# Kernel optimization log

Hardware: AMD Instinct MI355X
Metric: run time of the kernel (lower is better)

Reference implementation:

```python
import jax, jax.numpy as jnp
from jax import lax
import numpy as np

B, T, C_IN, H, W = 2, 4, 128, 64, 64
D_MODEL, N_Q, N_POINTS, PATCH, N_LAYERS = 256, 300, 8, 3, 6


def _sine_pos(Hh, Ww, d, temperature=10000.0):
    # mask is all-False, so cumsum of ones -> arange(1..H)/H * 2pi
    two_pi = 2.0 * np.pi
    yn = (jnp.arange(1, Hh + 1, dtype=jnp.float32) / (Hh + 1e-6)) * two_pi
    xn = (jnp.arange(1, Ww + 1, dtype=jnp.float32) / (Ww + 1e-6)) * two_pi
    q = d // 4
    i = jnp.arange(q, dtype=jnp.float32)
    dim_t = temperature ** (2.0 * jnp.floor(i / 2.0) / q)
    py = yn[:, None] / dim_t
    px = xn[:, None] / dim_t
    py = jnp.stack([jnp.sin(py), jnp.cos(py)], axis=-1).reshape(Hh, 2 * q)
    px = jnp.stack([jnp.sin(px), jnp.cos(px)], axis=-1).reshape(Ww, 2 * q)
    pos = jnp.concatenate([
        jnp.broadcast_to(py[:, None, :], (Hh, Ww, 2 * q)),
        jnp.broadcast_to(px[None, :, :], (Hh, Ww, 2 * q)),
    ], axis=-1)
    return jnp.transpose(pos, (2, 0, 1))  # [d,H,W]


def _sample_scale(fmap, ref, ps):
    # fmap [B,C,h,w]; ref [B,nQ,nP,2] in [0,1]. Bilinear grid_sample,
    # padding_mode='border', align_corners=True -> direct gather (no replication).
    Bc, C, h, w = fmap.shape
    half = (ps - 1) / 2.0
    off = jnp.linspace(-half, half, ps, dtype=jnp.float32)
    oy, ox = jnp.meshgrid(off, off, indexing='ij')  # [ps,ps]
    gx = ref[..., 0, None, None] * 2.0 - 1.0 + ox * (2.0 / w)  # [B,nQ,nP,ps,ps]
    gy = ref[..., 1, None, None] * 2.0 - 1.0 + oy * (2.0 / h)
    x = jnp.clip((gx + 1.0) * 0.5 * (w - 1), 0.0, w - 1.0)
    y = jnp.clip((gy + 1.0) * 0.5 * (h - 1), 0.0, h - 1.0)
    x0 = jnp.floor(x); y0 = jnp.floor(y)
    wx = x - x0; wy = y - y0
    x0i = x0.astype(jnp.int32); y0i = y0.astype(jnp.int32)
    x1i = jnp.minimum(x0i + 1, w - 1); y1i = jnp.minimum(y0i + 1, h - 1)

    def per_b(fb, y0b, x0b, y1b, x1b, wxb, wyb):
        v00 = fb[:, y0b, x0b]  # [C,nQ,nP,ps,ps]
        v01 = fb[:, y0b, x1b]
        v10 = fb[:, y1b, x0b]
        v11 = fb[:, y1b, x1b]
        return (v00 * (1 - wxb) * (1 - wyb) + v01 * wxb * (1 - wyb)
                + v10 * (1 - wxb) * wyb + v11 * wxb * wyb)

    out = jax.vmap(per_b)(fmap, y0i, x0i, y1i, x1i, wx, wy)  # [B,C,nQ,nP,ps,ps]
    return jnp.transpose(out, (0, 2, 3, 4, 5, 1))  # [B,nQ,nP,ps,ps,C]


def reference(feat, pred_boxes_init, w_tf, b_tf, w_in, b_in, w_lat, b_lat, w_sm, b_sm,
              q_embed, q_pos, Wq, bq, Wo, bo, Wp1, bp1, Wp2, bp2,
              w_r1, b_r1, w_r2, b_r2, w_b1, b_b1, w_b2, b_b2, w_cls, b_cls):
    Bb, Tt, Cin, Hh, Ww = feat.shape
    d = w_in.shape[0]
    nP = w_r2.shape[0] // 2
    ps = int(round((Wp1.shape[-1] // d) ** 0.5))
    # temporal fuse: Conv3d kernel (3,1,1), padding (1,0,0)
    x = lax.conv_general_dilated(jnp.transpose(feat, (0, 2, 1, 3, 4)), w_tf,
                                 (1, 1, 1), [(1, 1), (0, 0), (0, 0)],
                                 dimension_numbers=('NCDHW', 'OIDHW', 'NCDHW'))
    x = x + b_tf[None, :, None, None, None]
    x = x.mean(axis=2)  # [B,Cin,H,W]
    x = jnp.einsum('bchw,dc->bdhw', x, w_in) + b_in[None, :, None, None]
    x = x + _sine_pos(Hh, Ww, d)[None]
    # FPN over scales {1,2,4}: avg_pool -> 1x1 lateral -> 3x3 smooth
    feats = []
    for i, s in enumerate((1, 2, 4)):
        xi = x if s == 1 else x.reshape(Bb, d, Hh // s, s, Ww // s, s).mean(axis=(3, 5))
        xi = jnp.einsum('bchw,oc->bohw', xi, w_lat[i]) + b_lat[i][None, :, None, None]
        xi = lax.conv_general_dilated(xi, w_sm[i], (1, 1), [(1, 1), (1, 1)],
                                      dimension_numbers=('NCHW', 'OIHW', 'NCHW'))
        xi = xi + b_sm[i][None, :, None, None]
        feats.append(xi)
    nQ = q_embed.shape[0]
    queries = jnp.broadcast_to((q_embed + q_pos)[None], (Bb, nQ, d))
    boxes = pred_boxes_init
    inv_sqrt_d = 1.0 / float(np.sqrt(d))
    for l in range(Wq.shape[0]):
        h1 = jax.nn.relu(jnp.einsum('bqd,od->bqo', queries, w_r1) + b_r1)
        ro = jnp.tanh(jnp.einsum('bqd,od->bqo', h1, w_r2) + b_r2)
        ro = ro.reshape(Bb, nQ, nP, 2) * 0.5
        ref = jnp.clip(boxes[:, :, None, :2] + ro, 0.0, 1.0)
        sampled = jnp.concatenate([_sample_scale(f, ref, ps) for f in feats], axis=2)
        sampled = sampled[:, :, :nP]  # truncate multi-scale concat back to nP
        flat = sampled.reshape(Bb, nQ, nP, ps * ps * d)
        pv = jax.nn.relu(jnp.einsum('bqpi,oi->bqpo', flat, Wp1[l]) + bp1[l])
        pv = jnp.einsum('bqpd,od->bqpo', pv, Wp2[l]) + bp2[l]
        kv = pv.mean(axis=2)  # [B,nP_q,d] -> [B,nQ,d]
        q = jnp.einsum('bqd,od->bqo', queries, Wq[l]) + bq[l]
        attn = jax.nn.softmax(jnp.einsum('bqd,bkd->bqk', q, kv) * inv_sqrt_d, axis=-1)
        out = jnp.einsum('bqk,bkd->bqd', attn, kv)
        queries = queries + (jnp.einsum('bqd,od->bqo', out, Wo[l]) + bo[l])
        hb = jax.nn.relu(jnp.einsum('bqd,od->bqo', queries, w_b1) + b_b1)
        delta = jax.nn.sigmoid(jnp.einsum('bqd,od->bqo', hb, w_b2) + b_b2)
        boxes = jnp.clip(boxes + 0.1 * jnp.tanh(delta - 0.5), 0.0, 1.0)
    logits = (jnp.einsum('bqd,od->bqo', queries, w_cls) + b_cls)[..., 0]
    return logits, boxes


def setup_inputs() -> dict:
    key = jax.random.key(0)
    keys = iter(jax.random.split(key, 48))

    def nrm(shape, s=0.02):
        return jax.random.normal(next(keys), shape, dtype=jnp.float32) * s

    inp = {
        'feat': jax.random.normal(next(keys), (B, T, C_IN, H, W), dtype=jnp.float32),
        'pred_boxes_init': jax.random.uniform(next(keys), (B, N_Q, 4), dtype=jnp.float32),
        'w_tf': nrm((C_IN, C_IN, 3, 1, 1)), 'b_tf': jnp.zeros((C_IN,), jnp.float32),
        'w_in': nrm((D_MODEL, C_IN)), 'b_in': jnp.zeros((D_MODEL,), jnp.float32),
        'w_lat': nrm((3, D_MODEL, D_MODEL)), 'b_lat': jnp.zeros((3, D_MODEL), jnp.float32),
        'w_sm': nrm((3, D_MODEL, D_MODEL, 3, 3)), 'b_sm': jnp.zeros((3, D_MODEL), jnp.float32),
        'q_embed': nrm((N_Q, D_MODEL), 1.0), 'q_pos': nrm((N_Q, D_MODEL), 1.0),
        'Wq': nrm((N_LAYERS, D_MODEL, D_MODEL)), 'bq': jnp.zeros((N_LAYERS, D_MODEL), jnp.float32),
        'Wo': nrm((N_LAYERS, D_MODEL, D_MODEL)), 'bo': jnp.zeros((N_LAYERS, D_MODEL), jnp.float32),
        'Wp1': nrm((N_LAYERS, D_MODEL, PATCH * PATCH * D_MODEL)), 'bp1': jnp.zeros((N_LAYERS, D_MODEL), jnp.float32),
        'Wp2': nrm((N_LAYERS, D_MODEL, D_MODEL)), 'bp2': jnp.zeros((N_LAYERS, D_MODEL), jnp.float32),
        'w_r1': nrm((D_MODEL, D_MODEL)), 'b_r1': jnp.zeros((D_MODEL,), jnp.float32),
        'w_r2': nrm((2 * N_POINTS, D_MODEL)), 'b_r2': jnp.zeros((2 * N_POINTS,), jnp.float32),
        'w_b1': nrm((D_MODEL, D_MODEL)), 'b_b1': jnp.zeros((D_MODEL,), jnp.float32),
        'w_b2': nrm((4, D_MODEL)), 'b_b2': jnp.zeros((4,), jnp.float32),
        'w_cls': nrm((1, D_MODEL)), 'b_cls': jnp.zeros((1,), jnp.float32),
    }
    return inp
```

## Files before the change

### kernel.cpp

```cpp
#include <hip/hip_runtime.h>
#include <hip/hip_bf16.h>
#include <math.h>

#define BB 2
#define TT 4
#define CIN 128
#define DM 256
#define NQ 300
#define NP 8
#define PS 3
#define NL 6
#define HW 4096
#define KP 2304

typedef __attribute__((ext_vector_type(8))) short short8;
typedef __attribute__((ext_vector_type(4))) short short4_t;
typedef __attribute__((ext_vector_type(4))) float f32x4;
typedef unsigned short ushort_t;

static __device__ __forceinline__ ushort_t f2bf(float f) {
  __hip_bfloat16 h = __float2bfloat16(f);
  return *reinterpret_cast<ushort_t*>(&h);
}
static __device__ __forceinline__ float bf2f(ushort_t u) {
  return __uint_as_float(((unsigned)u) << 16);
}

__global__ void k_prep(const float* __restrict__ w_in, const float* __restrict__ w_lat,
                       const float* __restrict__ w_b1,
                       const float* __restrict__ w_r1, const float* __restrict__ Wp1,
                       ushort_t* __restrict__ win_bf, ushort_t* __restrict__ wlat_bf,
                       ushort_t* __restrict__ wb1_bf,
                       ushort_t* __restrict__ wr1_bf, ushort_t* __restrict__ wp1_bf,
                       const float* __restrict__ w_tf, ushort_t* __restrict__ tct,
                       const float* __restrict__ w_sm, ushort_t* __restrict__ wsm_bf,
                       const float* __restrict__ Wp2, const float* __restrict__ Wo,
                       const float* __restrict__ bq, const float* __restrict__ bp2,
                       const float* __restrict__ bo,
                       float* __restrict__ bqt, float* __restrict__ bfuse,
                       uint4* __restrict__ x2p_zero,
                       const float* __restrict__ b_tf, const float* __restrict__ b_in,
                       float* __restrict__ bias_comb,
                       const float* __restrict__ qe, const float* __restrict__ qp,
                       const float* __restrict__ pb, float* __restrict__ queries,
                       ushort_t* __restrict__ qbf, float* __restrict__ boxes,
                       const float* __restrict__ feat, ushort_t* __restrict__ featT) {
  __shared__ float ldsF[64][65];
  float* bt = &ldsF[0][0];
  int b = blockIdx.x, t = threadIdx.x;
  if (b < 3680) {
    int i = b * 256 + t;
    const float* s; ushort_t* d; int base;
    if (i < 8192)         { s = w_in;  d = win_bf;  base = 0; }
    else if (i < 24576)   { s = w_lat; d = wlat_bf; base = 8192; }
    else if (i < 40960)   { s = w_b1;  d = wb1_bf;  base = 24576; }
    else if (i < 57344)   { s = w_r1;  d = wr1_bf;  base = 40960; }
    else                  { s = Wp1;   d = wp1_bf;  base = 57344; }
    int j = i - base;
    float4 v = ((const float4*)s)[j];
    d[j * 4 + 0] = f2bf(v.x);
    d[j * 4 + 1] = f2bf(v.y);
    d[j * 4 + 2] = f2bf(v.z);
    d[j * 4 + 3] = f2bf(v.w);
  } else if (b < 3936) {
    int i = (b - 3680) * 256 + t;
    int k = i >> 7, c = i & 127;
    int u = k >> 7, ci = k & 127;
    const float* wp = w_tf + ((size_t)(c * 128 + ci)) * 3;
    float w0 = wp[0], w1 = wp[1], w2 = wp[2];
    float coef = (u == 0) ? (w0 + w1) : (u == 3) ? (w1 + w2) : (w0 + w1 + w2);
    tct[(size_t)k * 128 + c] = f2bf(0.25f * coef);
  } else if (b < 6240) {
    int i = (b - 3936) * 256 + t;
    int n = i / KP;
    int r = i - n * KP;
    int tp = r >> 8, c = r & 255;
    wsm_bf[i] = f2bf(w_sm[((size_t)(n * 256 + c)) * 9 + tp]);
  } else if (b < 6252) {
    int i = (b - 6240) * 256 + t;
    if (i < 1536) {
      int l = i >> 8, d = i & 255;
      float a = 0.f;
      for (int o = 0; o < 256; ++o)
        a += bq[l * 256 + o] * Wp2[((size_t)(l * 256 + o)) * 256 + d];
      bqt[i] = a;
    } else {
      int j = i - 1536;
      int l = j >> 8, o2 = j & 255;
      float a = bo[l * 256 + o2];
      for (int o = 0; o < 256; ++o)
        a += bp2[l * 256 + o] * Wo[((size_t)(l * 256 + o2)) * 256 + o];
      bfuse[j] = a;
    }
  } else if (b < 7341) {
    int j = (b - 6252) * 256 + t;
    if (j < 278784) x2p_zero[j] = make_uint4(0u, 0u, 0u, 0u);
  } else if (b < 7342) {
    int d = t;
    if (d < 128) bt[d] = b_tf[d];
    __syncthreads();
    float a = b_in[d];
    for (int c = 0; c < 128; ++c) a += w_in[d * 128 + c] * bt[c];
    bias_comb[d] = a;
  } else if (b < 7942) {
    int i = (b - 7342) * 256 + t;
    if (i < BB * NQ * DM) {
      int rd = i % (NQ * DM);
      float v = qe[rd] + qp[rd];
      queries[i] = v;
      qbf[i] = f2bf(v);
    }
    if (i < BB * NQ * 4) boxes[i] = pb[i];
  } else {
    int idx = b - 7942;
    int gs = idx & 127;
    int k0 = (idx >> 7) * 64;
    int bb = gs >> 6;
    int s0 = (gs & 63) * 64;
    int kk = t >> 2, sc0 = (t & 3) * 16;
    {
      int k = k0 + kk;
      int u = k >> 7, ci = k & 127;
      const float* src = feat + (((size_t)(bb * 4 + u) * 128 + ci) << 12) + s0 + sc0;
#pragma unroll
      for (int j = 0; j < 4; ++j) {
        float4 v = *(const float4*)(src + j * 4);
        ldsF[kk][sc0 + j * 4 + 0] = v.x;
        ldsF[kk][sc0 + j * 4 + 1] = v.y;
        ldsF[kk][sc0 + j * 4 + 2] = v.z;
        ldsF[kk][sc0 + j * 4 + 3] = v.w;
      }
    }
    __syncthreads();
#pragma unroll
    for (int p = 0; p < 2; ++p) {
      int idx2 = p * 256 + t;
      int s_l = idx2 >> 3, kc = (idx2 & 7) * 8;
      short8 v;
#pragma unroll
      for (int j = 0; j < 8; ++j) v[j] = (short)f2bf(ldsF[kc + j][s_l]);
      *(short8*)(featT + (size_t)(bb * 4096 + s0 + s_l) * 512 + k0 + kc) = v;
    }
  }
}

__global__ __launch_bounds__(256) void k_wcompose(const float* __restrict__ Wp2,
                                                  const float* __restrict__ Wq,
                                                  const float* __restrict__ Wo,
                                                  ushort_t* __restrict__ wqt,
                                                  ushort_t* __restrict__ wfuseT) {
  __shared__ ushort_t As[64 * 36];
  __shared__ ushort_t Bs[64 * 36];
  int z = blockIdx.z, l = z % 6;
  const float* Asrc = Wp2 + (size_t)l * 65536;
  const float* Bsrc = ((z < 6) ? Wq : Wo) + (size_t)l * 65536;
  ushort_t* C = ((z < 6) ? wqt : wfuseT) + (size_t)l * 65536;
  bool btr = (z < 6);
  int tid = threadIdx.x;
  int bm = blockIdx.x * 64, bn = blockIdx.y * 64;
  int w = tid >> 6, lane = tid & 63;
  int wm = (w & 1) * 32, wn = (w >> 1) * 32;
  int q = lane >> 4, ml = lane & 15;
  f32x4 acc[2][2] = {};
  int oo = tid >> 3, mg = (tid & 7) * 8;
  int nr = tid >> 2, kg = (tid & 3) * 8;
  for (int k0 = 0; k0 < 256; k0 += 32) {
    {
      const float* sp = Asrc + (size_t)(k0 + oo) * 256 + bm + mg;
      float4 f0 = *(const float4*)sp;
      float4 f1 = *(const float4*)(sp + 4);
      ushort_t* dst = As + oo;
      dst[(mg + 0) * 36] = f2bf(f0.x); dst[(mg + 1) * 36] = f2bf(f0.y);
      dst[(mg + 2) * 36] = f2bf(f0.z); dst[(mg + 3) * 36] = f2bf(f0.w);
      dst[(mg + 4) * 36] = f2bf(f1.x); dst[(mg + 5) * 36] = f2bf(f1.y);
      dst[(mg + 6) * 36] = f2bf(f1.z); dst[(mg + 7) * 36] = f2bf(f1.w);
    }
    if (btr) {
      const float* sp = Bsrc + (size_t)(k0 + oo) * 256 + bn + mg;
      float4 f0 = *(const float4*)sp;
      float4 f1 = *(const float4*)(sp + 4);
      ushort_t* dst = Bs + oo;
      dst[(mg + 0) * 36] = f2bf(f0.x); dst[(mg + 1) * 36] = f2bf(f0.y);
      dst[(mg + 2) * 36] = f2bf(f0.z); dst[(mg + 3) * 36] = f2bf(f0.w);
      dst[(mg + 4) * 36] = f2bf(f1.x); dst[(mg + 5) * 36] = f2bf(f1.y);
      dst[(mg + 6) * 36] = f2bf(f1.z); dst[(mg + 7) * 36] = f2bf(f1.w);
    } else {
      const float* sp = Bsrc + (size_t)(bn + nr) * 256 + k0 + kg;
      float4 f0 = *(const float4*)sp;
      float4 f1 = *(const float4*)(sp + 4);
      short8 v;
      v[0] = (short)f2bf(f0.x); v[1] = (short)f2bf(f0.y);
      v[2] = (short)f2bf(f0.z); v[3] = (short)f2bf(f0.w);
      v[4] = (short)f2bf(f1.x); v[5] = (short)f2bf(f1.y);
      v[6] = (short)f2bf(f1.z); v[7] = (short)f2bf(f1.w);
      *(short8*)(Bs + nr * 36 + kg) = v;
    }
    __syncthreads();
    short8 a0 = *(const short8*)(As + (wm + ml) * 36 + q * 8);
    short8 a1 = *(const short8*)(As + (wm + 16 + ml) * 36 + q * 8);
    short8 b0 = *(const short8*)(Bs + (wn + ml) * 36 + q * 8);
    short8 b1 = *(const short8*)(Bs + (wn + 16 + ml) * 36 + q * 8);
    acc[0][0] = __builtin_amdgcn_mfma_f32_16x16x32_bf16(a0, b0, acc[0][0], 0, 0, 0);
    acc[0][1] = __builtin_amdgcn_mfma_f32_16x16x32_bf16(a0, b1, acc[0][1], 0, 0, 0);
    acc[1][0] = __builtin_amdgcn_mfma_f32_16x16x32_bf16(a1, b0, acc[1][0], 0, 0, 0);
    acc[1][1] = __builtin_amdgcn_mfma_f32_16x16x32_bf16(a1, b1, acc[1][1], 0, 0, 0);
    __syncthreads();
  }
#pragma unroll
  for (int i = 0; i < 2; ++i)
#pragma unroll
    for (int j = 0; j < 2; ++j) {
      int cn = bn + wn + j * 16 + ml;
#pragma unroll
      for (int r = 0; r < 4; ++r) {
        int rm = bm + wm + i * 16 + q * 4 + r;
        C[(size_t)rm * 256 + cn] = f2bf(acc[i][j][r]);
      }
    }
}

__global__ __launch_bounds__(256) void k_feat2(const ushort_t* __restrict__ featT,
                                               const ushort_t* __restrict__ wcomb,
                                               const float* __restrict__ biasc,
                                               ushort_t* __restrict__ xcl) {
  __shared__ ushort_t As[32 * 72];
  __shared__ ushort_t Bs[64 * 72];
  __shared__ float dimt_s[256];
  int tid = threadIdx.x;
  {
    int dd = tid & 127;
    int ii = dd >> 1;
    dimt_s[tid] = powf(10000.0f, (2.0f * (float)(ii >> 1)) / 64.0f);
  }
  int bm = blockIdx.x * 32, bn = blockIdx.y * 64;
  int w = tid >> 6, lane = tid & 63;
  int wm = (w & 1) * 16, wn = (w >> 1) * 32;
  int q = lane >> 4, ml = lane & 15;
  int sra = tid >> 3, sca = (tid & 7) * 8;
  int srb = tid >> 2, scb = (tid & 3) * 16;
  const ushort_t* Ag = featT + (size_t)(bm + sra) * 512 + sca;
  const ushort_t* Wg = wcomb + (size_t)(bn + srb) * 512 + scb;
  f32x4 acc[2] = {};
  short8 av = *(const short8*)Ag;
  short8 wv0 = *(const short8*)Wg;
  short8 wv1 = *(const short8*)(Wg + 8);
  for (int k0 = 0; k0 < 512; k0 += 64) {
    *(short8*)(As + sra * 72 + sca) = av;
    *(short8*)(Bs + srb * 72 + scb) = wv0;
    *(short8*)(Bs + srb * 72 + scb + 8) = wv1;
    __syncthreads();
    if (k0 + 64 < 512) {
      av = *(const short8*)(Ag + k0 + 64);
      wv0 = *(const short8*)(Wg + k0 + 64);
      wv1 = *(const short8*)(Wg + k0 + 72);
    }
#pragma unroll
    for (int h = 0; h < 2; ++h) {
      int kc = h * 32 + q * 8;
      short8 a = *(const short8*)(As + (wm + ml) * 72 + kc);
      short8 b0 = *(const short8*)(Bs + (wn + ml) * 72 + kc);
      short8 b1 = *(const short8*)(Bs + (wn + 16 + ml) * 72 + kc);
      acc[0] = __builtin_amdgcn_mfma_f32_16x16x32_bf16(a, b0, acc[0], 0, 0, 0);
      acc[1] = __builtin_amdgcn_mfma_f32_16x16x32_bf16(a, b1, acc[1], 0, 0, 0);
    }
    __syncthreads();
  }
  const float FKT = 6.28318530717958647692f / 64.000001f;
#pragma unroll
  for (int j = 0; j < 2; ++j) {
    int cn = bn + wn + j * 16 + ml;
    float dimt = dimt_s[cn];
    float bC = biasc[cn];
    bool isx = cn >= 128;
    bool isc = cn & 1;
#pragma unroll
    for (int r = 0; r < 4; ++r) {
      int rm = bm + wm + q * 4 + r;
      int s = rm & 4095;
      int y = s >> 6, x = s & 63;
      float ang = (float)((isx ? x : y) + 1) * FKT / dimt;
      float pos = isc ? cosf(ang) : sinf(ang);
      xcl[(size_t)rm * 256 + cn] = f2bf(acc[j][r] + bC + pos);
    }
  }
}

template <int ACT, int OUTMODE, int MG>
__global__ __launch_bounds__(256) void k_gemm_bf16(const ushort_t* __restrict__ A,
                                                   const ushort_t* __restrict__ W,
                                                   const float* __restrict__ bias,
                                                   const float* __restrict__ res,
                                                   float* __restrict__ Cf,
                                                   ushort_t* __restrict__ Cb,
                                                   int M, int N, int K,
                                                   const ushort_t* __restrict__ W2,
                                                   const float* __restrict__ bias2,
                                                   const ushort_t* __restrict__ W3,
                                                   const float* __restrict__ bias3) {
  __shared__ ushort_t As[64 * 72];
  __shared__ ushort_t Bs[64 * 72];
  int tid = threadIdx.x;
  int bm = blockIdx.x * 64, bn = blockIdx.y * 64;
  int w = tid >> 6, lane = tid & 63;
  int wm = (w & 1) * 32, wn = (w >> 1) * 32;
  int q = lane >> 4, ml = lane & 15;
  f32x4 acc[2][2] = {};
  int srow = tid >> 2, scol = (tid & 3) * 16;
  int ga = bm + srow;
  if (MG) ga = min(ga, M - 1);
  const ushort_t* Ag = A + (size_t)ga * K + scol;
  const ushort_t* Wg;
  if (OUTMODE == 7) {
    int seg = bn >> 8;
    const ushort_t* Wb = (seg == 0) ? W : ((seg == 1) ? W2 : W3);
    Wg = Wb + (size_t)((bn & 255) + srow) * K + scol;
  } else if (OUTMODE == 4) {
    const ushort_t* Wb = (bn < 256) ? W : W2;
    Wg = Wb + (size_t)((bn & 255) + srow) * K + scol;
  } else {
    Wg = W + (size_t)(bn + srow) * K + scol;
  }
  short8 av0 = *(const short8*)(Ag);
  short8 av1 = *(const short8*)(Ag + 8);
  short8 wv0 = *(const short8*)(Wg);
  short8 wv1 = *(const short8*)(Wg + 8);
  for (int k0 = 0; k0 < K; k0 += 64) {
    *(short8*)(As + srow * 72 + scol) = av0;
    *(short8*)(As + srow * 72 + scol + 8) = av1;
    *(short8*)(Bs + srow * 72 + scol) = wv0;
    *(short8*)(Bs + srow * 72 + scol + 8) = wv1;
    __syncthreads();
    if (k0 + 64 < K) {
      av0 = *(const short8*)(Ag + k0 + 64);
      av1 = *(const short8*)(Ag + k0 + 72);
      wv0 = *(const short8*)(Wg + k0 + 64);
      wv1 = *(const short8*)(Wg + k0 + 72);
    }
#pragma unroll
    for (int h = 0; h < 2; ++h) {
      int kc = h * 32 + q * 8;
      short8 a0 = *(const short8*)(As + (wm + ml) * 72 + kc);
      short8 a1 = *(const short8*)(As + (wm + 16 + ml) * 72 + kc);
      short8 b0 = *(const short8*)(Bs + (wn + ml) * 72 + kc);
      short8 b1 = *(const short8*)(Bs + (wn + 16 + ml) * 72 + kc);
      acc[0][0] = __builtin_amdgcn_mfma_f32_16x16x32_bf16(a0, b0, acc[0][0], 0, 0, 0);
      acc[0][1] = __builtin_amdgcn_mfma_f32_16x16x32_bf16(a0, b1, acc[0][1], 0, 0, 0);
      acc[1][0] = __builtin_amdgcn_mfma_f32_16x16x32_bf16(a1, b0, acc[1][0], 0, 0, 0);
      acc[1][1] = __builtin_amdgcn_mfma_f32_16x16x32_bf16(a1, b1, acc[1][1], 0, 0, 0);
    }
    __syncthreads();
  }
#pragma unroll
  for (int i = 0; i < 2; ++i) {
#pragma unroll
    for (int j = 0; j < 2; ++j) {
      int cn = bn + wn + j * 16 + ml;
      float bsv;
      if (OUTMODE == 7) {
        int seg = cn >> 8;
        bsv = ((seg == 0) ? bias : ((seg == 1) ? bias2 : bias3))[cn & 255];
      } else if (OUTMODE == 4) {
        bsv = ((cn < 256) ? bias : bias2)[cn & 255];
      } else {
        bsv = bias ? bias[cn] : 0.f;
      }
#pragma unroll
      for (int r = 0; r < 4; ++r) {
        int rm = bm + wm + i * 16 + q * 4 + r;
        if (MG && rm >= M) continue;
        float v = acc[i][j][r] + bsv;
        if (OUTMODE == 0) {
          if (ACT == 1) v = fmaxf(v, 0.f);
          Cf[(size_t)rm * N + cn] = v;
        } else if (OUTMODE == 1) {
          int b = rm >> 12, rem = rm & 4095;
          int y = rem >> 6, xx = rem & 63;
          Cb[(((size_t)(b * 66 + y + 1)) * 66 + xx + 1) * 256 + cn] = f2bf(v);
        } else if (OUTMODE == 4) {
          if (cn < 256) Cf[(size_t)rm * 256 + cn] = fmaxf(v, 0.f);
          else Cb[(size_t)rm * 256 + (cn & 255)] = f2bf(v);
        } else if (OUTMODE == 6) {
          Cb[(size_t)rm * N + cn] = f2bf(v);
        } else if (OUTMODE == 7) {
          if (cn < 256) Cf[(size_t)rm * 256 + cn] = fmaxf(v, 0.f);
          else if (cn < 512) ((float*)Cb)[(size_t)rm * 256 + (cn & 255)] = fmaxf(v, 0.f);
          else ((ushort_t*)res)[(size_t)rm * 256 + (cn & 255)] = f2bf(v);
        }
      }
    }
  }
}

__global__ __launch_bounds__(256) void k_wp1_split(const ushort_t* __restrict__ A,
                                                   const ushort_t* __restrict__ W,
                                                   ushort_t* __restrict__ part) {
  __shared__ ushort_t As[64 * 72];
  __shared__ ushort_t Bs[64 * 72];
  int tid = threadIdx.x;
  int bm = blockIdx.x * 64, bn = blockIdx.y * 64;
  int kz = blockIdx.z * 768;
  int w = tid >> 6, lane = tid & 63;
  int wm = (w & 1) * 32, wn = (w >> 1) * 32;
  int q = lane >> 4, ml = lane & 15;
  int srow = tid >> 2, scol = (tid & 3) * 16;
  const ushort_t* Ag = A + (size_t)(bm + srow) * KP + kz + scol;
  const ushort_t* Wg = W + (size_t)(bn + srow) * KP + kz + scol;
  f32x4 acc[2][2] = {};
  short8 av0 = *(const short8*)(Ag);
  short8 av1 = *(const short8*)(Ag + 8);
  short8 wv0 = *(const short8*)(Wg);
  short8 wv1 = *(const short8*)(Wg + 8);
  for (int k0 = 0; k0 < 768; k0 += 64) {
    *(short8*)(As + srow * 72 + scol) = av0;
    *(short8*)(As + srow * 72 + scol + 8) = av1;
    *(short8*)(Bs + srow * 72 + scol) = wv0;
    *(short8*)(Bs + srow * 72 + scol + 8) = wv1;
    __syncthreads();
    if (k0 + 64 < 768) {
      av0 = *(const short8*)(Ag + k0 + 64);
      av1 = *(const short8*)(Ag + k0 + 72);
      wv0 = *(const short8*)(Wg + k0 + 64);
      wv1 = *(const short8*)(Wg + k0 + 72);
    }
#pragma unroll
    for (int h = 0; h < 2; ++h) {
      int kc = h * 32 + q * 8;
      short8 a0 = *(const short8*)(As + (wm + ml) * 72 + kc);
      short8 a1 = *(const short8*)(As + (wm + 16 + ml) * 72 + kc);
      short8 b0 = *(const short8*)(Bs + (wn + ml) * 72 + kc);
      short8 b1 = *(const short8*)(Bs + (wn + 16 + ml) * 72 + kc);
      acc[0][0] = __builtin_amdgcn_mfma_f32_16x16x32_bf16(a0, b0, acc[0][0], 0, 0, 0);
      acc[0][1] = __builtin_amdgcn_mfma_f32_16x16x32_bf16(a0, b1, acc[0][1], 0, 0, 0);
      acc[1][0] = __builtin_amdgcn_mfma_f32_16x16x32_bf16(a1, b0, acc[1][0], 0, 0, 0);
      acc[1][1] = __builtin_amdgcn_mfma_f32_16x16x32_bf16(a1, b1, acc[1][1], 0, 0, 0);
    }
    __syncthreads();
  }
  ushort_t* pz = part + (size_t)blockIdx.z * 4800 * 256;
#pragma unroll
  for (int i = 0; i < 2; ++i)
#pragma unroll
    for (int j = 0; j < 2; ++j) {
      int cn = bn + wn + j * 16 + ml;
#pragma unroll
      for (int r = 0; r < 4; ++r) {
        int rm = bm + wm + i * 16 + q * 4 + r;
        pz[(size_t)rm * 256 + cn] = f2bf(acc[i][j][r]);
      }
    }
}

__global__ __launch_bounds__(256) void k_wp1_reduce(const ushort_t* __restrict__ part,
                                                    const float* __restrict__ bias,
                                                    ushort_t* __restrict__ pvm) {
  int row = blockIdx.x;
  int d = threadIdx.x;
  float b = bias[d];
  float s = 0.f;
#pragma unroll
  for (int p = 0; p < 8; ++p) {
    size_t idx = (size_t)(row * 8 + p) * 256 + d;
    float v = bf2f(part[idx]) + bf2f(part[idx + (size_t)4800 * 256]) +
              bf2f(part[idx + (size_t)2 * 4800 * 256]) + b;
    s += fmaxf(v, 0.f);
  }
  pvm[(size_t)row * 256 + d] = f2bf(s * 0.125f);
}

__global__ __launch_bounds__(256) void k_conv3(const ushort_t* __restrict__ x2p,
                                               const ushort_t* __restrict__ wsm,
                                               const float* __restrict__ bsm,
                                               ushort_t* __restrict__ fcl) {
  __shared__ ushort_t As[32 * 72];
  __shared__ ushort_t Bs[64 * 72];
  int tid = threadIdx.x;
  int bm = blockIdx.x * 32, bn = blockIdx.y * 64;
  int w = tid >> 6, lane = tid & 63;
  int wm = (w & 1) * 16, wn = (w >> 1) * 32;
  int q = lane >> 4, ml = lane & 15;
  int sra = tid >> 3, sca = (tid & 7) * 8;
  int srb = tid >> 2, scb = (tid & 3) * 16;
  int sA = bm + sra;
  int b = sA >> 12, rem = sA & 4095;
  size_t pbase = ((size_t)(b * 66 + (rem >> 6)) * 66 + (rem & 63)) * 256;
  const ushort_t* Wg = wsm + (size_t)(bn + srb) * KP + scb;
  auto loadA = [&](int k0) {
    int ka = k0 + sca;
    int t9 = ka >> 8;
    int ky = t9 / 3, kx = t9 - ky * 3;
    return *(const short8*)(x2p + pbase + (size_t)(ky * 66 + kx) * 256 + (ka & 255));
  };
  f32x4 acc[2] = {};
  short8 av = loadA(0);
  short8 wv0 = *(const short8*)(Wg);
  short8 wv1 = *(const short8*)(Wg + 8);
  for (int k0 = 0; k0 < KP; k0 += 64) {
    *(short8*)(As + sra * 72 + sca) = av;
    *(short8*)(Bs + srb * 72 + scb) = wv0;
    *(short8*)(Bs + srb * 72 + scb + 8) = wv1;
    __syncthreads();
    if (k0 + 64 < KP) {
      av = loadA(k0 + 64);
      wv0 = *(const short8*)(Wg + k0 + 64);
      wv1 = *(const short8*)(Wg + k0 + 72);
    }
#pragma unroll
    for (int h = 0; h < 2; ++h) {
      int kc = h * 32 + q * 8;
      short8 a = *(const short8*)(As + (wm + ml) * 72 + kc);
      short8 b0 = *(const short8*)(Bs + (wn + ml) * 72 + kc);
      short8 b1 = *(const short8*)(Bs + (wn + 16 + ml) * 72 + kc);
      acc[0] = __builtin_amdgcn_mfma_f32_16x16x32_bf16(a, b0, acc[0], 0, 0, 0);
      acc[1] = __builtin_amdgcn_mfma_f32_16x16x32_bf16(a, b1, acc[1], 0, 0, 0);
    }
    __syncthreads();
  }
#pragma unroll
  for (int j = 0; j < 2; ++j) {
    int cn = bn + wn + j * 16 + ml;
    float bsv = bsm[cn];
#pragma unroll
    for (int r = 0; r < 4; ++r) {
      int rm = bm + wm + q * 4 + r;
      fcl[(size_t)rm * 256 + cn] = f2bf(acc[j][r] + bsv);
    }
  }
}

__global__ __launch_bounds__(256) void k_sample(const ushort_t* __restrict__ fcl,
                                                const float* __restrict__ h1,
                                                const float* __restrict__ w_r2,
                                                const float* __restrict__ b_r2,
                                                const float* __restrict__ boxesIn,
                                                float* __restrict__ boxesOut,
                                                const float* __restrict__ hb,
                                                const float* __restrict__ w_b2,
                                                const float* __restrict__ b_b2,
                                                ushort_t* __restrict__ flat) {
  __shared__ float pr[8];
  __shared__ float bc2[2];
  __shared__ float nb2[2];
  int blk = blockIdx.x;
  int row = blk >> 3, p = blk & 7;
  int b = row / NQ;
  int tid = threadIdx.x;
  int w = tid >> 6, lane = tid & 63;
  if (hb) {
    float4 hv = *(const float4*)(hb + (size_t)row * 256 + lane * 4);
    float4 wv = *(const float4*)(w_b2 + (size_t)w * 256 + lane * 4);
    float aa = hv.x * wv.x + hv.y * wv.y + hv.z * wv.z + hv.w * wv.w;
#pragma unroll
    for (int s = 32; s > 0; s >>= 1) aa += __shfl_down(aa, s, 64);
    if (lane == 0) {
      aa += b_b2[w];
      float delta = 1.0f / (1.0f + expf(-aa));
      float v = boxesIn[row * 4 + w] + 0.1f * tanhf(delta - 0.5f);
      v = fminf(fmaxf(v, 0.f), 1.f);
      if (w < 2) nb2[w] = v;
      if (p == 0) boxesOut[row * 4 + w] = v;
    }
  } else if (tid < 2) {
    nb2[tid] = boxesIn[row * 4 + tid];
  }
  float h = h1[(size_t)row * 256 + tid];
  float px = h * w_r2[(size_t)(2 * p) * 256 + tid];
  float py = h * w_r2[(size_t)(2 * p + 1) * 256 + tid];
#pragma unroll
  for (int s = 32; s > 0; s >>= 1) {
    px += __shfl_down(px, s, 64);
    py += __shfl_down(py, s, 64);
  }
  if (lane == 0) { pr[w * 2] = px; pr[w * 2 + 1] = py; }
  __syncthreads();
  if (tid == 0) {
    float sx = pr[0] + pr[2] + pr[4] + pr[6] + b_r2[2 * p];
    float sy = pr[1] + pr[3] + pr[5] + pr[7] + b_r2[2 * p + 1];
    float rx = nb2[0] + 0.5f * tanhf(sx);
    float ry = nb2[1] + 0.5f * tanhf(sy);
    bc2[0] = fminf(fmaxf(rx, 0.f), 1.f);
    bc2[1] = fminf(fmaxf(ry, 0.f), 1.f);
  }
  __syncthreads();
  float rx = bc2[0], ry = bc2[1];
  int c = tid;
  const ushort_t* fb = fcl + (size_t)b * HW * DM;
  ushort_t* op = flat + (size_t)blk * KP;
#pragma unroll
  for (int jy = 0; jy < 3; ++jy) {
    float yy = (ry + (float)(jy - 1) * (1.0f / 64.0f)) * 63.0f;
    yy = fminf(fmaxf(yy, 0.f), 63.0f);
    float y0f = floorf(yy);
    float wy = yy - y0f;
    int y0 = (int)y0f;
    int y1 = min(y0 + 1, 63);
#pragma unroll
    for (int jx = 0; jx < 3; ++jx) {
      float xx = (rx + (float)(jx - 1) * (1.0f / 64.0f)) * 63.0f;
      xx = fminf(fmaxf(xx, 0.f), 63.0f);
      float x0f = floorf(xx);
      float wx = xx - x0f;
      int x0 = (int)x0f;
      int x1 = min(x0 + 1, 63);
      float v00 = bf2f(fb[(y0 * 64 + x0) * DM + c]);
      float v01 = bf2f(fb[(y0 * 64 + x1) * DM + c]);
      float v10 = bf2f(fb[(y1 * 64 + x0) * DM + c]);
      float v11 = bf2f(fb[(y1 * 64 + x1) * DM + c]);
      float v = v00 * (1.f - wx) * (1.f - wy) + v01 * wx * (1.f - wy) +
                v10 * (1.f - wx) * wy + v11 * wx * wy;
      op[(jy * 3 + jx) * DM + c] = f2bf(v);
    }
  }
}

__global__ __launch_bounds__(256) void k_attn(const ushort_t* __restrict__ qt,
                                              const ushort_t* __restrict__ pvm,
                                              const ushort_t* __restrict__ wfT,
                                              const float* __restrict__ bfuse_l,
                                              float* __restrict__ queries,
                                              ushort_t* __restrict__ qbf) {
  __shared__ float qs[256];
  __shared__ float sc[512];
  __shared__ float red[256];
  __shared__ float pr4[1024];
  int row = blockIdx.x;
  int b = row / NQ;
  int tid = threadIdx.x;
  qs[tid] = bf2f(qt[(size_t)row * DM + tid]);
  __syncthreads();
  const ushort_t* kvB = pvm + (size_t)b * NQ * DM;
#pragma unroll
  for (int s2 = 0; s2 < 2; ++s2) {
    int k = tid + s2 * 256;
    float v = -1e30f;
    if (k < NQ) {
      const ushort_t* kp = kvB + (size_t)k * DM;
      float a = 0.f;
#pragma unroll
      for (int d = 0; d < 256; d += 8) {
        short8 k8 = *(const short8*)(kp + d);
        const float* qd = qs + d;
        a += bf2f((ushort_t)k8[0]) * qd[0];
        a += bf2f((ushort_t)k8[1]) * qd[1];
        a += bf2f((ushort_t)k8[2]) * qd[2];
        a += bf2f((ushort_t)k8[3]) * qd[3];
        a += bf2f((ushort_t)k8[4]) * qd[4];
        a += bf2f((ushort_t)k8[5]) * qd[5];
        a += bf2f((ushort_t)k8[6]) * qd[6];
        a += bf2f((ushort_t)k8[7]) * qd[7];
      }
      v = a * (1.0f / 16.0f);
    }
    sc[k] = v;
  }
  __syncthreads();
  red[tid] = fmaxf(sc[tid], sc[tid + 256]);
  __syncthreads();
  for (int st = 128; st > 0; st >>= 1) {
    if (tid < st) red[tid] = fmaxf(red[tid], red[tid + st]);
    __syncthreads();
  }
  float mx = red[0];
  __syncthreads();
  float e0 = (tid < NQ) ? expf(sc[tid] - mx) : 0.f;
  float e1 = (tid + 256 < NQ) ? expf(sc[tid + 256] - mx) : 0.f;
  sc[tid] = e0;
  sc[tid + 256] = e1;
  red[tid] = e0 + e1;
  __syncthreads();
  for (int st = 128; st > 0; st >>= 1) {
    if (tid < st) red[tid] += red[tid + st];
    __syncthreads();
  }
  float inv = 1.0f / red[0];
  __syncthreads();
  float acc = 0.f;
#pragma unroll 4
  for (int k = 0; k < NQ; ++k)
    acc += sc[k] * bf2f(kvB[(size_t)k * DM + tid]);
  qs[tid] = acc * inv;
  __syncthreads();
  int oq = (tid & 63) * 4, dq = (tid >> 6) * 64;
  float a0 = 0.f, a1 = 0.f, a2 = 0.f, a3 = 0.f;
  const ushort_t* wp = wfT + (size_t)dq * 256 + oq;
#pragma unroll 8
  for (int dd = 0; dd < 64; ++dd) {
    float cc = qs[dq + dd];
    short4_t wv = *(const short4_t*)(wp + (size_t)dd * 256);
    a0 += cc * bf2f((ushort_t)wv[0]);
    a1 += cc * bf2f((ushort_t)wv[1]);
    a2 += cc * bf2f((ushort_t)wv[2]);
    a3 += cc * bf2f((ushort_t)wv[3]);
  }
  float* pb4 = pr4 + (tid >> 6) * 256 + oq;
  pb4[0] = a0; pb4[1] = a1; pb4[2] = a2; pb4[3] = a3;
  __syncthreads();
  float v = pr4[tid] + pr4[256 + tid] + pr4[512 + tid] + pr4[768 + tid] +
            bfuse_l[tid] + queries[(size_t)row * DM + tid];
  queries[(size_t)row * DM + tid] = v;
  qbf[(size_t)row * DM + tid] = f2bf(v);
}

__global__ __launch_bounds__(256) void k_boxf(const float* __restrict__ hb,
                                              const float* __restrict__ w_b2,
                                              const float* __restrict__ b_b2,
                                              float* __restrict__ boxes,
                                              int last,
                                              const float* __restrict__ queries,
                                              const float* __restrict__ w_cls,
                                              const float* __restrict__ b_cls,
                                              float* __restrict__ out) {
  __shared__ float nb[4];
  int row = blockIdx.x;
  int tid = threadIdx.x;
  int j = tid >> 6, lane = tid & 63;
  float4 hv = *(const float4*)(hb + (size_t)row * 256 + lane * 4);
  float4 wv = *(const float4*)(w_b2 + (size_t)j * 256 + lane * 4);
  float aa = hv.x * wv.x + hv.y * wv.y + hv.z * wv.z + hv.w * wv.w;
#pragma unroll
  for (int s = 32; s > 0; s >>= 1) aa += __shfl_down(aa, s, 64);
  if (lane == 0) {
    aa += b_b2[j];
    float delta = 1.0f / (1.0f + expf(-aa));
    float v = boxes[row * 4 + j] + 0.1f * tanhf(delta - 0.5f);
    v = fminf(fmaxf(v, 0.f), 1.f);
    boxes[row * 4 + j] = v;
    nb[j] = v;
  }
  if (last) {
    __syncthreads();
    if (j == 0) {
      float4 qv = *(const float4*)(queries + (size_t)row * 256 + lane * 4);
      float4 cv = *(const float4*)(w_cls + lane * 4);
      float a2 = qv.x * cv.x + qv.y * cv.y + qv.z * cv.z + qv.w * cv.w;
#pragma unroll
      for (int s = 32; s > 0; s >>= 1) a2 += __shfl_down(a2, s, 64);
      if (lane == 0) out[row] = a2 + b_cls[0];
    } else if (j == 1 && lane < 4) {
      out[600 + row * 4 + lane] = nb[lane];
    }
  }
}

extern "C" void kernel_launch(void* const* d_in, const int* in_sizes, int n_in,
                              void* d_out, int out_size, void* d_ws, size_t ws_size,
                              hipStream_t stream) {
  const float* feat   = (const float*)d_in[0];
  const float* pb     = (const float*)d_in[1];
  const float* w_tf   = (const float*)d_in[2];
  const float* b_tf   = (const float*)d_in[3];
  const float* w_in   = (const float*)d_in[4];
  const float* b_in   = (const float*)d_in[5];
  const float* w_lat  = (const float*)d_in[6];
  const float* b_lat  = (const float*)d_in[7];
  const float* w_sm   = (const float*)d_in[8];
  const float* b_sm   = (const float*)d_in[9];
  const float* q_embed= (const float*)d_in[10];
  const float* q_pos  = (const float*)d_in[11];
  const float* Wq     = (const float*)d_in[12];
  const float* bq     = (const float*)d_in[13];
  const float* Wo     = (const float*)d_in[14];
  const float* bo     = (const float*)d_in[15];
  const float* Wp1    = (const float*)d_in[16];
  const float* bp1    = (const float*)d_in[17];
  const float* Wp2    = (const float*)d_in[18];
  const float* bp2    = (const float*)d_in[19];
  const float* w_r1   = (const float*)d_in[20];
  const float* b_r1   = (const float*)d_in[21];
  const float* w_r2   = (const float*)d_in[22];
  const float* b_r2   = (const float*)d_in[23];
  const float* w_b1   = (const float*)d_in[24];
  const float* b_b1   = (const float*)d_in[25];
  const float* w_b2   = (const float*)d_in[26];
  const float* b_b2   = (const float*)d_in[27];
  const float* w_cls  = (const float*)d_in[28];
  const float* b_cls  = (const float*)d_in[29];
  float* out = (float*)d_out;

  float* ws = (float*)d_ws;
  size_t off = 0;
  auto alloc = [&](size_t n) { float* p = ws + off; off += n; return p; };
  ushort_t* flat    = (ushort_t*)alloc(5529600);
  ushort_t* part    = (ushort_t*)alloc(1843200);
  ushort_t* featT   = (ushort_t*)alloc(2097152);
  ushort_t* xcl     = (ushort_t*)alloc(1048576);
  ushort_t* x2p     = (ushort_t*)alloc(1115136);
  ushort_t* fcl     = (ushort_t*)alloc(1048576);
  ushort_t* wcomb   = (ushort_t*)alloc(65536);
  ushort_t* tct     = (ushort_t*)alloc(32768);
  ushort_t* win_bf  = (ushort_t*)alloc(16384);
  float*    biasc   = alloc(256);
  ushort_t* wlat_bf = (ushort_t*)alloc(32768);
  ushort_t* wsm_bf  = (ushort_t*)alloc(294912);
  ushort_t* wp1_bf  = (ushort_t*)alloc(1769472);
  ushort_t* wb1_bf  = (ushort_t*)alloc(32768);
  ushort_t* wr1_bf  = (ushort_t*)alloc(32768);
  ushort_t* wqt_bf  = (ushort_t*)alloc(196608);
  ushort_t* wfuseT  = (ushort_t*)alloc(196608);
  float*    bqt     = alloc(1536);
  float*    bfuse   = alloc(1536);
  float* queries = alloc(153600);
  ushort_t* qbf  = (ushort_t*)alloc(76800);
  float* h1      = alloc(153600);
  ushort_t* qt   = (ushort_t*)alloc(76800);
  float* hb      = alloc(153600);
  ushort_t* pvm  = (ushort_t*)alloc(76800);
  float* boxesA  = alloc(2400);
  float* boxesB  = alloc(2400);
  (void)ws_size; (void)in_sizes; (void)n_in; (void)out_size;

  k_prep<<<8966, 256, 0, stream>>>(w_in, w_lat, w_b1, w_r1, Wp1,
                                   win_bf, wlat_bf, wb1_bf, wr1_bf, wp1_bf,
                                   w_tf, tct, w_sm, wsm_bf,
                                   Wp2, Wo, bq, bp2, bo, bqt, bfuse,
                                   (uint4*)x2p, b_tf, b_in, biasc,
                                   q_embed, q_pos, pb, queries, qbf, boxesA,
                                   feat, featT);
  k_gemm_bf16<0, 6, 0><<<dim3(4, 8), 256, 0, stream>>>(win_bf, tct, nullptr, nullptr,
                                                       nullptr, wcomb, 256, 512, 128,
                                                       nullptr, nullptr, nullptr, nullptr);
  k_wcompose<<<dim3(4, 4, 12), 256, 0, stream>>>(Wp2, Wq, Wo, wqt_bf, wfuseT);

  k_feat2<<<dim3(256, 4), 256, 0, stream>>>(featT, wcomb, biasc, xcl);
  k_gemm_bf16<0, 1, 0><<<dim3(128, 4), 256, 0, stream>>>(xcl, wlat_bf, b_lat, nullptr,
                                                         nullptr, x2p, BB * HW, 256, 256,
                                                         nullptr, nullptr, nullptr, nullptr);
  k_conv3<<<dim3(256, 4), 256, 0, stream>>>(x2p, wsm_bf, b_sm, fcl);

  const int M6 = BB * NQ;
  const int Mp = BB * NQ * NP;
  dim3 g600w((M6 + 63) / 64, 8);
  dim3 g600m((M6 + 63) / 64, 12);
  dim3 gsk(Mp / 64, 4, 3);

  k_gemm_bf16<0, 4, 1><<<g600w, 256, 0, stream>>>(qbf, wr1_bf, b_r1, nullptr, h1,
                                                  qt, M6, 512, 256,
                                                  wqt_bf, bqt, nullptr, nullptr);
  float* bcur = boxesA;
  float* bnext = boxesB;
  for (int l = 0; l < NL; ++l) {
    const float* hbp = (l == 0) ? nullptr : hb;
    k_sample<<<Mp, 256, 0, stream>>>(fcl, h1, w_r2, b_r2, bcur, bnext,
                                     hbp, w_b2, b_b2, flat);
    if (l > 0) { float* tmp = bcur; bcur = bnext; bnext = tmp; }
    k_wp1_split<<<gsk, 256, 0, stream>>>(flat, wp1_bf + (size_t)l * 256 * KP, part);
    k_wp1_reduce<<<600, 256, 0, stream>>>(part, bp1 + (size_t)l * DM, pvm);
    k_attn<<<M6, 256, 0, stream>>>(qt, pvm, wfuseT + (size_t)l * 65536,
                                   bfuse + l * 256, queries, qbf);
    int ln = (l + 1) % NL;
    k_gemm_bf16<0, 7, 1><<<g600m, 256, 0, stream>>>(qbf, wb1_bf, b_b1, (const float*)qt,
                                                    hb, (ushort_t*)h1, M6, 768, 256,
                                                    wr1_bf, b_r1,
                                                    wqt_bf + (size_t)ln * 65536,
                                                    bqt + ln * 256);
  }
  k_boxf<<<M6, 256, 0, stream>>>(hb, w_b2, b_b2, bcur, 1,
                                 queries, w_cls, b_cls, out);
}
```

Baseline: 673.9 us.

## Fold lateral 1x1 conv into 3x3 smoothing weights and vectorize sampling

Composes the lateral 1x1 projection weights into each tap of the 3x3 smoothing conv (new k_convcompose), so the separate lateral GEMM launch and its intermediate buffer go away. The lateral bias is propagated through a per-tap bias table applied with border-aware masking in the conv epilogue, and k_feat2 writes straight into the padded layout. Separately, k_sample now has each thread handle four channels with vector loads and splits the nine patch positions across warps. Composing the weights rounds an extra bf16 product, which may change numerics slightly.

Measured after the change: 694.8 us. 1.03x slower.

```diff
diff --git a/kernel.cpp b/kernel.cpp
--- a/kernel.cpp
+++ b/kernel.cpp
@@ -26,10 +26,10 @@
   return __uint_as_float(((unsigned)u) << 16);
 }
 
-__global__ void k_prep(const float* __restrict__ w_in, const float* __restrict__ w_lat,
+__global__ void k_prep(const float* __restrict__ w_in,
                        const float* __restrict__ w_b1,
                        const float* __restrict__ w_r1, const float* __restrict__ Wp1,
-                       ushort_t* __restrict__ win_bf, ushort_t* __restrict__ wlat_bf,
+                       ushort_t* __restrict__ win_bf,
                        ushort_t* __restrict__ wb1_bf,
                        ushort_t* __restrict__ wr1_bf, ushort_t* __restrict__ wp1_bf,
                        const float* __restrict__ w_tf, ushort_t* __restrict__ tct,
@@ -38,7 +38,8 @@
                        const float* __restrict__ bq, const float* __restrict__ bp2,
                        const float* __restrict__ bo,
                        float* __restrict__ bqt, float* __restrict__ bfuse,
-                       uint4* __restrict__ x2p_zero,
+                       const float* __restrict__ b_lat, float* __restrict__ T9,
+                       uint4* __restrict__ xclp_zero,
                        const float* __restrict__ b_tf, const float* __restrict__ b_in,
                        float* __restrict__ bias_comb,
                        const float* __restrict__ qe, const float* __restrict__ qp,
@@ -48,62 +49,68 @@
   __shared__ float ldsF[64][65];
   float* bt = &ldsF[0][0];
   int b = blockIdx.x, t = threadIdx.x;
-  if (b < 3680) {
+  if (b < 3616) {
     int i = b * 256 + t;
     const float* s; ushort_t* d; int base;
     if (i < 8192)         { s = w_in;  d = win_bf;  base = 0; }
-    else if (i < 24576)   { s = w_lat; d = wlat_bf; base = 8192; }
-    else if (i < 40960)   { s = w_b1;  d = wb1_bf;  base = 24576; }
-    else if (i < 57344)   { s = w_r1;  d = wr1_bf;  base = 40960; }
-    else                  { s = Wp1;   d = wp1_bf;  base = 57344; }
+    else if (i < 24576)   { s = w_b1;  d = wb1_bf;  base = 8192; }
+    else if (i < 40960)   { s = w_r1;  d = wr1_bf;  base = 24576; }
+    else                  { s = Wp1;   d = wp1_bf;  base = 40960; }
     int j = i - base;
     float4 v = ((const float4*)s)[j];
     d[j * 4 + 0] = f2bf(v.x);
     d[j * 4 + 1] = f2bf(v.y);
     d[j * 4 + 2] = f2bf(v.z);
     d[j * 4 + 3] = f2bf(v.w);
-  } else if (b < 3936) {
-    int i = (b - 3680) * 256 + t;
+  } else if (b < 3872) {
+    int i = (b - 3616) * 256 + t;
     int k = i >> 7, c = i & 127;
     int u = k >> 7, ci = k & 127;
     const float* wp = w_tf + ((size_t)(c * 128 + ci)) * 3;
     float w0 = wp[0], w1 = wp[1], w2 = wp[2];
     float coef = (u == 0) ? (w0 + w1) : (u == 3) ? (w1 + w2) : (w0 + w1 + w2);
     tct[(size_t)k * 128 + c] = f2bf(0.25f * coef);
-  } else if (b < 6240) {
-    int i = (b - 3936) * 256 + t;
+  } else if (b < 6176) {
+    int i = (b - 3872) * 256 + t;
     int n = i / KP;
     int r = i - n * KP;
     int tp = r >> 8, c = r & 255;
     wsm_bf[i] = f2bf(w_sm[((size_t)(n * 256 + c)) * 9 + tp]);
-  } else if (b < 6252) {
-    int i = (b - 6240) * 256 + t;
+  } else if (b < 6197) {
+    int i = (b - 6176) * 256 + t;
     if (i < 1536) {
       int l = i >> 8, d = i & 255;
       float a = 0.f;
       for (int o = 0; o < 256; ++o)
         a += bq[l * 256 + o] * Wp2[((size_t)(l * 256 + o)) * 256 + d];
       bqt[i] = a;
-    } else {
+    } else if (i < 3072) {
       int j = i - 1536;
       int l = j >> 8, o2 = j & 255;
       float a = bo[l * 256 + o2];
       for (int o = 0; o < 256; ++o)
         a += bp2[l * 256 + o] * Wo[((size_t)(l * 256 + o2)) * 256 + o];
       bfuse[j] = a;
-    }
-  } else if (b < 7341) {
-    int j = (b - 6252) * 256 + t;
-    if (j < 278784) x2p_zero[j] = make_uint4(0u, 0u, 0u, 0u);
-  } else if (b < 7342) {
+    } else {
+      int j = i - 3072;
+      int tap = j >> 8, n = j & 255;
+      float a = 0.f;
+      for (int c = 0; c < 256; ++c)
+        a += w_sm[((size_t)(n * 256 + c)) * 9 + tap] * b_lat[c];
+      T9[j] = a;
+    }
+  } else if (b < 7286) {
+    int j = (b - 6197) * 256 + t;
+    if (j < 278784) xclp_zero[j] = make_uint4(0u, 0u, 0u, 0u);
+  } else if (b < 7287) {
     int d = t;
     if (d < 128) bt[d] = b_tf[d];
     __syncthreads();
     float a = b_in[d];
     for (int c = 0; c < 128; ++c) a += w_in[d * 128 + c] * bt[c];
     bias_comb[d] = a;
-  } else if (b < 7942) {
-    int i = (b - 7342) * 256 + t;
+  } else if (b < 7887) {
+    int i = (b - 7287) * 256 + t;
     if (i < BB * NQ * DM) {
       int rd = i % (NQ * DM);
       float v = qe[rd] + qp[rd];
@@ -112,7 +119,7 @@
     }
     if (i < BB * NQ * 4) boxes[i] = pb[i];
   } else {
-    int idx = b - 7942;
+    int idx = b - 7887;
     int gs = idx & 127;
     int k0 = (idx >> 7) * 64;
     int bb = gs >> 6;
@@ -219,10 +226,70 @@
     }
 }
 
+__global__ __launch_bounds__(256) void k_convcompose(const ushort_t* __restrict__ wsm,
+                                                     const float* __restrict__ w_lat,
+                                                     ushort_t* __restrict__ w2) {
+  __shared__ ushort_t As[64 * 72];
+  __shared__ ushort_t Bs[64 * 72];
+  int tap = blockIdx.z;
+  int tid = threadIdx.x;
+  int bm = blockIdx.x * 64, bn = blockIdx.y * 64;
+  int w = tid >> 6, lane = tid & 63;
+  int wm = (w & 1) * 32, wn = (w >> 1) * 32;
+  int q = lane >> 4, ml = lane & 15;
+  f32x4 acc[2][2] = {};
+  int srow = tid >> 2, scol = (tid & 3) * 16;
+  const ushort_t* Ag = wsm + (size_t)(bm + srow) * KP + tap * 256 + scol;
+  int ko = tid >> 2, cg = (tid & 3) * 16;
+  for (int k0 = 0; k0 < 256; k0 += 64) {
+    short8 a0 = *(const short8*)(Ag + k0);
+    short8 a1 = *(const short8*)(Ag + k0 + 8);
+    *(short8*)(As + srow * 72 + scol) = a0;
+    *(short8*)(As + srow * 72 + scol + 8) = a1;
+    {
+      const float* sp = w_lat + (size_t)(k0 + ko) * 256 + bn + cg;
+      ushort_t* dst = Bs + ko;
+#pragma unroll
+      for (int jj = 0; jj < 4; ++jj) {
+        float4 f = *(const float4*)(sp + jj * 4);
+        dst[(cg + jj * 4 + 0) * 72] = f2bf(f.x);
+        dst[(cg + jj * 4 + 1) * 72] = f2bf(f.y);
+        dst[(cg + jj * 4 + 2) * 72] = f2bf(f.z);
+        dst[(cg + jj * 4 + 3) * 72] = f2bf(f.w);
+      }
+    }
+    __syncthreads();
+#pragma unroll
+    for (int h = 0; h < 2; ++h) {
+      int kc = h * 32 + q * 8;
+      short8 fa0 = *(const short8*)(As + (wm + ml) * 72 + kc);
+      short8 fa1 = *(const short8*)(As + (wm + 16 + ml) * 72 + kc);
+      short8 fb0 = *(const short8*)(Bs + (wn + ml) * 72 + kc);
+      short8 fb1 = *(const short8*)(Bs + (wn + 16 + ml) * 72 + kc);
+      acc[0][0] = __builtin_amdgcn_mfma_f32_16x16x32_bf16(fa0, fb0, acc[0][0], 0, 0, 0);
+      acc[0][1] = __builtin_amdgcn_mfma_f32_16x16x32_bf16(fa0, fb1, acc[0][1], 0, 0, 0);
+      acc[1][0] = __builtin_amdgcn_mfma_f32_16x16x32_bf16(fa1, fb0, acc[1][0], 0, 0, 0);
+      acc[1][1] = __builtin_amdgcn_mfma_f32_16x16x32_bf16(fa1, fb1, acc[1][1], 0, 0, 0);
+    }
+    __syncthreads();
+  }
+#pragma unroll
+  for (int i = 0; i < 2; ++i)
+#pragma unroll
+    for (int j = 0; j < 2; ++j) {
+      int cn = bn + wn + j * 16 + ml;
+#pragma unroll
+      for (int r = 0; r < 4; ++r) {
+        int rm = bm + wm + i * 16 + q * 4 + r;
+        w2[(size_t)rm * KP + tap * 256 + cn] = f2bf(acc[i][j][r]);
+      }
+    }
+}
+
 __global__ __launch_bounds__(256) void k_feat2(const ushort_t* __restrict__ featT,
                                                const ushort_t* __restrict__ wcomb,
                                                const float* __restrict__ biasc,
-                                               ushort_t* __restrict__ xcl) {
+                                               ushort_t* __restrict__ xclp) {
   __shared__ ushort_t As[32 * 72];
   __shared__ ushort_t Bs[64 * 72];
   __shared__ float dimt_s[256];
@@ -276,11 +343,12 @@
 #pragma unroll
     for (int r = 0; r < 4; ++r) {
       int rm = bm + wm + q * 4 + r;
-      int s = rm & 4095;
-      int y = s >> 6, x = s & 63;
+      int bb = rm >> 12, rem = rm & 4095;
+      int y = rem >> 6, x = rem & 63;
       float ang = (float)((isx ? x : y) + 1) * FKT / dimt;
       float pos = isc ? cosf(ang) : sinf(ang);
-      xcl[(size_t)rm * 256 + cn] = f2bf(acc[j][r] + bC + pos);
+      xclp[(((size_t)(bb * 66 + y + 1)) * 66 + x + 1) * 256 + cn] =
+          f2bf(acc[j][r] + bC + pos);
     }
   }
 }
@@ -372,10 +440,6 @@
         if (OUTMODE == 0) {
           if (ACT == 1) v = fmaxf(v, 0.f);
           Cf[(size_t)rm * N + cn] = v;
-        } else if (OUTMODE == 1) {
-          int b = rm >> 12, rem = rm & 4095;
-          int y = rem >> 6, xx = rem & 63;
-          Cb[(((size_t)(b * 66 + y + 1)) * 66 + xx + 1) * 256 + cn] = f2bf(v);
         } else if (OUTMODE == 4) {
           if (cn < 256) Cf[(size_t)rm * 256 + cn] = fmaxf(v, 0.f);
           else Cb[(size_t)rm * 256 + (cn & 255)] = f2bf(v);
@@ -467,13 +531,17 @@
   pvm[(size_t)row * 256 + d] = f2bf(s * 0.125f);
 }
 
-__global__ __launch_bounds__(256) void k_conv3(const ushort_t* __restrict__ x2p,
+__global__ __launch_bounds__(256) void k_conv3(const ushort_t* __restrict__ xclp,
                                                const ushort_t* __restrict__ wsm,
                                                const float* __restrict__ bsm,
+                                               const float* __restrict__ T9,
                                                ushort_t* __restrict__ fcl) {
   __shared__ ushort_t As[32 * 72];
   __shared__ ushort_t Bs[64 * 72];
+  __shared__ float T9s[9][256];
   int tid = threadIdx.x;
+#pragma unroll
+  for (int tap = 0; tap < 9; ++tap) T9s[tap][tid] = T9[tap * 256 + tid];
   int bm = blockIdx.x * 32, bn = blockIdx.y * 64;
   int w = tid >> 6, lane = tid & 63;
   int wm = (w & 1) * 16, wn = (w >> 1) * 32;
@@ -488,7 +556,7 @@
     int ka = k0 + sca;
     int t9 = ka >> 8;
     int ky = t9 / 3, kx = t9 - ky * 3;
-    return *(const short8*)(x2p + pbase + (size_t)(ky * 66 + kx) * 256 + (ka & 255));
+    return *(const short8*)(xclp + pbase + (size_t)(ky * 66 + kx) * 256 + (ka & 255));
   };
   f32x4 acc[2] = {};
   short8 av = loadA(0);
@@ -522,7 +590,20 @@
 #pragma unroll
     for (int r = 0; r < 4; ++r) {
       int rm = bm + wm + q * 4 + r;
-      fcl[(size_t)rm * 256 + cn] = f2bf(acc[j][r] + bsv);
+      int sy = (rm >> 6) & 63, sx = rm & 63;
+      float bias = bsv;
+#pragma unroll
+      for (int ky = 0; ky < 3; ++ky) {
+        int iy = sy + ky - 1;
+        if (iy < 0 || iy > 63) continue;
+#pragma unroll
+        for (int kx = 0; kx < 3; ++kx) {
+          int ix = sx + kx - 1;
+          if (ix < 0 || ix > 63) continue;
+          bias += T9s[ky * 3 + kx][cn];
+        }
+      }
+      fcl[(size_t)rm * 256 + cn] = f2bf(acc[j][r] + bias);
     }
   }
 }
@@ -582,33 +663,41 @@
   }
   __syncthreads();
   float rx = bc2[0], ry = bc2[1];
-  int c = tid;
   const ushort_t* fb = fcl + (size_t)b * HW * DM;
   ushort_t* op = flat + (size_t)blk * KP;
-#pragma unroll
-  for (int jy = 0; jy < 3; ++jy) {
+  int c4 = (tid & 63) * 4;
+  int g = tid >> 6;
+  int p0 = (g == 0) ? 0 : (1 + 2 * g);
+  int p1 = (g == 0) ? 3 : (3 + 2 * g);
+  for (int p9 = p0; p9 < p1; ++p9) {
+    int jy = (p9 >= 6) ? 2 : ((p9 >= 3) ? 1 : 0);
+    int jx = p9 - jy * 3;
     float yy = (ry + (float)(jy - 1) * (1.0f / 64.0f)) * 63.0f;
     yy = fminf(fmaxf(yy, 0.f), 63.0f);
     float y0f = floorf(yy);
     float wy = yy - y0f;
     int y0 = (int)y0f;
     int y1 = min(y0 + 1, 63);
-#pragma unroll
-    for (int jx = 0; jx < 3; ++jx) {
-      float xx = (rx + (float)(jx - 1) * (1.0f / 64.0f)) * 63.0f;
-      xx = fminf(fmaxf(xx, 0.f), 63.0f);
-      float x0f = floorf(xx);
-      float wx = xx - x0f;
-      int x0 = (int)x0f;
-      int x1 = min(x0 + 1, 63);
-      float v00 = bf2f(fb[(y0 * 64 + x0) * DM + c]);
-      float v01 = bf2f(fb[(y0 * 64 + x1) * DM + c]);
-      float v10 = bf2f(fb[(y1 * 64 + x0) * DM + c]);
-      float v11 = bf2f(fb[(y1 * 64 + x1) * DM + c]);
-      float v = v00 * (1.f - wx) * (1.f - wy) + v01 * wx * (1.f - wy) +
-                v10 * (1.f - wx) * wy + v11 * wx * wy;
-      op[(jy * 3 + jx) * DM + c] = f2bf(v);
-    }
+    float xx = (rx + (float)(jx - 1) * (1.0f / 64.0f)) * 63.0f;
+    xx = fminf(fmaxf(xx, 0.f), 63.0f);
+    float x0f = floorf(xx);
+    float wx = xx - x0f;
+    int x0 = (int)x0f;
+    int x1 = min(x0 + 1, 63);
+    short4_t v00 = *(const short4_t*)(fb + (y0 * 64 + x0) * DM + c4);
+    short4_t v01 = *(const short4_t*)(fb + (y0 * 64 + x1) * DM + c4);
+    short4_t v10 = *(const short4_t*)(fb + (y1 * 64 + x0) * DM + c4);
+    short4_t v11 = *(const short4_t*)(fb + (y1 * 64 + x1) * DM + c4);
+    short4_t ov;
+#pragma unroll
+    for (int jj = 0; jj < 4; ++jj) {
+      float v = bf2f((ushort_t)v00[jj]) * (1.f - wx) * (1.f - wy) +
+                bf2f((ushort_t)v01[jj]) * wx * (1.f - wy) +
+                bf2f((ushort_t)v10[jj]) * (1.f - wx) * wy +
+                bf2f((ushort_t)v11[jj]) * wx * wy;
+      ov[jj] = (short)f2bf(v);
+    }
+    *(short4_t*)(op + p9 * DM + c4) = ov;
   }
 }
 
@@ -782,15 +871,15 @@
   ushort_t* flat    = (ushort_t*)alloc(5529600);
   ushort_t* part    = (ushort_t*)alloc(1843200);
   ushort_t* featT   = (ushort_t*)alloc(2097152);
-  ushort_t* xcl     = (ushort_t*)alloc(1048576);
-  ushort_t* x2p     = (ushort_t*)alloc(1115136);
+  ushort_t* xclp    = (ushort_t*)alloc(1115136);
   ushort_t* fcl     = (ushort_t*)alloc(1048576);
   ushort_t* wcomb   = (ushort_t*)alloc(65536);
   ushort_t* tct     = (ushort_t*)alloc(32768);
   ushort_t* win_bf  = (ushort_t*)alloc(16384);
   float*    biasc   = alloc(256);
-  ushort_t* wlat_bf = (ushort_t*)alloc(32768);
   ushort_t* wsm_bf  = (ushort_t*)alloc(294912);
+  ushort_t* w2      = (ushort_t*)alloc(294912);
+  float*    T9f     = alloc(2304);
   ushort_t* wp1_bf  = (ushort_t*)alloc(1769472);
   ushort_t* wb1_bf  = (ushort_t*)alloc(32768);
   ushort_t* wr1_bf  = (ushort_t*)alloc(32768);
@@ -808,23 +897,22 @@
   float* boxesB  = alloc(2400);
   (void)ws_size; (void)in_sizes; (void)n_in; (void)out_size;
 
-  k_prep<<<8966, 256, 0, stream>>>(w_in, w_lat, w_b1, w_r1, Wp1,
-                                   win_bf, wlat_bf, wb1_bf, wr1_bf, wp1_bf,
+  k_prep<<<8911, 256, 0, stream>>>(w_in, w_b1, w_r1, Wp1,
+                                   win_bf, wb1_bf, wr1_bf, wp1_bf,
                                    w_tf, tct, w_sm, wsm_bf,
                                    Wp2, Wo, bq, bp2, bo, bqt, bfuse,
-                                   (uint4*)x2p, b_tf, b_in, biasc,
+                                   b_lat, T9f,
+                                   (uint4*)xclp, b_tf, b_in, biasc,
                                    q_embed, q_pos, pb, queries, qbf, boxesA,
                                    feat, featT);
   k_gemm_bf16<0, 6, 0><<<dim3(4, 8), 256, 0, stream>>>(win_bf, tct, nullptr, nullptr,
                                                        nullptr, wcomb, 256, 512, 128,
                                                        nullptr, nullptr, nullptr, nullptr);
   k_wcompose<<<dim3(4, 4, 12), 256, 0, stream>>>(Wp2, Wq, Wo, wqt_bf, wfuseT);
-
-  k_feat2<<<dim3(256, 4), 256, 0, stream>>>(featT, wcomb, biasc, xcl);
-  k_gemm_bf16<0, 1, 0><<<dim3(128, 4), 256, 0, stream>>>(xcl, wlat_bf, b_lat, nullptr,
-                                                         nullptr, x2p, BB * HW, 256, 256,
-                                                         nullptr, nullptr, nullptr, nullptr);
-  k_conv3<<<dim3(256, 4), 256, 0, stream>>>(x2p, wsm_bf, b_sm, fcl);
+  k_convcompose<<<dim3(4, 4, 9), 256, 0, stream>>>(wsm_bf, w_lat, w2);
+
+  k_feat2<<<dim3(256, 4), 256, 0, stream>>>(featT, wcomb, biasc, xclp);
+  k_conv3<<<dim3(256, 4), 256, 0, stream>>>(xclp, w2, b_sm, T9f, fcl);
 
   const int M6 = BB * NQ;
   const int Mp = BB * NQ * NP;
```
